# Performance work log

Measured on AMD Instinct MI355X. Metric: run time of the kernel, lower is better.

## Reference

```python
import jax, jax.numpy as jnp
import numpy as np

# pywt db4 decomposition low-pass filter
_DEC_LO = jnp.array([-0.010597401785069032, 0.0328830116668852, 0.030841381835560764,
                     -0.18703481171909309, -0.027983769416859854, 0.6308807679298589,
                     0.7148465705529157, 0.2303778133088965], dtype=jnp.float32)
_L = 8
_SIGN = jnp.where(jnp.arange(_L) % 2 == 0, -1.0, 1.0).astype(jnp.float32)
_DEC_HI = _SIGN * _DEC_LO[::-1]            # QMF: dec_hi[k] = (-1)^(k+1) dec_lo[L-1-k]
_REC_LO = _DEC_LO[::-1]
_REC_HI = _DEC_HI[::-1]
_LEVELS = 4


def _conv_valid(x, f):
    # x: [N, n]; true convolution (filter flipped), valid part
    k = f[::-1][None, None, :]
    return jax.lax.conv_general_dilated(x[:, None, :], k, (1,), 'VALID',
                                        dimension_numbers=('NCH', 'OIH', 'NCH'))[:, 0, :]


def _dwt(x):
    # one symmetric-mode DWT level; x: [N, n] -> (cA, cD) each [N, (n+L-1)//2]
    xp = jnp.pad(x, ((0, 0), (_L - 1, _L - 1)), mode='symmetric')
    return _conv_valid(xp, _DEC_LO)[:, 1::2], _conv_valid(xp, _DEC_HI)[:, 1::2]


def _idwt(a, d):
    # inverse DWT level; a,d: [N, m] -> [N, 2m-L+2]
    m = a.shape[-1]
    up_a = jnp.zeros((a.shape[0], 2 * m - 1), a.dtype).at[:, ::2].set(a)
    up_d = jnp.zeros((d.shape[0], 2 * m - 1), d.dtype).at[:, ::2].set(d)
    y = (_conv_valid(jnp.pad(up_a, ((0, 0), (_L - 1, _L - 1))), _REC_LO)
         + _conv_valid(jnp.pad(up_d, ((0, 0), (_L - 1, _L - 1))), _REC_HI))
    return y[:, _L - 2: y.shape[-1] - (_L - 2)]


def _wavelet_compress(x, level):
    # batched equivalent of the per-(b,c) pywt wavedec/threshold/waverec loop
    B, C, T = x.shape
    a = x.reshape(B * C, T)
    details = []
    for _ in range(_LEVELS):
        a, d = _dwt(a)
        details.append(d)
    thr = level * jnp.std(a, axis=-1, keepdims=True)  # np.std (ddof=0) of approx coeffs per row
    hard = lambda c: jnp.where(jnp.abs(c) < thr, jnp.zeros((), c.dtype), c)
    a = hard(a)
    for d in reversed(details):
        d = hard(d)
        if a.shape[-1] > d.shape[-1]:
            a = a[:, :d.shape[-1]]  # pywt waverec length alignment
        a = _idwt(a, d)
    if a.shape[-1] >= T:
        a = a[:, :T]
    else:
        a = jnp.pad(a, ((0, 0), (0, T - a.shape[-1])))
    return a.reshape(B, C, T)


def _spectral_distortion(x, key, freq_mask_prob=0.3, time_mask_prob=0.3):
    T = x.shape[-1]
    k1, k2, k3, k4 = jax.random.split(key, 4)
    X = jnp.fft.fft(x, axis=-1)
    mag, ph = jnp.abs(X), jnp.angle(X)
    idx = jnp.arange(T)
    fw = int(0.1 * T)
    f0 = jax.random.randint(k2, (), 0, T - fw)
    apply_f = jax.random.uniform(k1, ()) < freq_mask_prob
    fmask = apply_f & (idx >= f0) & (idx < f0 + fw)
    mag = mag * jnp.where(fmask, 0.1, 1.0).astype(mag.dtype)
    xd = jnp.fft.ifft(mag * jnp.exp(1j * ph), axis=-1).real.astype(x.dtype)
    tw = int(0.05 * T)
    t0 = jax.random.randint(k4, (), 0, T - tw)
    apply_t = jax.random.uniform(k3, ()) < time_mask_prob
    tmask = apply_t & (idx >= t0) & (idx < t0 + tw)
    return xd * jnp.where(tmask, 0.1, 1.0).astype(x.dtype)


def _add_noise(x, key, noise_std=0.02):
    # torch.std is unbiased -> ddof=1
    noise = jax.random.normal(key, x.shape, x.dtype) * noise_std * jnp.std(x, axis=-1, keepdims=True, ddof=1)
    return x + noise


def setup_inputs() -> dict:
    key = jax.random.key(0)
    x = jax.random.normal(key, (64, 64, 4096), dtype=jnp.float32)
    return {"x": x}


def reference(x):
    compression_level = 0.5  # fixed draw from compression_levels for determinism
    kd, kn, kcd, kcn = jax.random.split(jax.random.key(42), 4)
    compressed = _wavelet_compress(x, compression_level)
    distorted = _spectral_distortion(x, kd)
    noisy = _add_noise(x, kn)
    comb = _wavelet_compress(x, compression_level * 0.5)
    comb = _spectral_distortion(comb, kcd)
    comb = _add_noise(comb, kcn)
    # views: original, compressed, distorted, noisy, combined
    return (x, compressed, distorted, noisy, comb)
```

## Files before the change

### kernel.cpp

```cpp
#include <hip/hip_runtime.h>
#include <stdint.h>

#define T_LEN 4096
#define N_ROWS 4096
#define N_ELEM (4096u * 4096u)
#define PD(i) ((i) + ((i) >> 5))

__constant__ float c_DEC_LO[8] = {
  -0.010597401785069032f, 0.0328830116668852f, 0.030841381835560764f,
  -0.18703481171909309f, -0.027983769416859854f, 0.6308807679298589f,
   0.7148465705529157f, 0.2303778133088965f };
__constant__ float c_DEC_HI[8] = {
  -0.2303778133088965f, 0.7148465705529157f, -0.6308807679298589f,
  -0.027983769416859854f, 0.18703481171909309f, 0.030841381835560764f,
  -0.0328830116668852f, -0.010597401785069032f };

#define RL0 0.2303778133088965f
#define RL1 0.7148465705529157f
#define RL2 0.6308807679298589f
#define RL3 (-0.027983769416859854f)
#define RL4 (-0.18703481171909309f)
#define RL5 0.030841381835560764f
#define RL6 0.0328830116668852f
#define RL7 (-0.010597401785069032f)
#define RH0 (-0.010597401785069032f)
#define RH1 (-0.0328830116668852f)
#define RH2 0.030841381835560764f
#define RH3 0.18703481171909309f
#define RH4 (-0.027983769416859854f)
#define RH5 (-0.6308807679298589f)
#define RH6 0.7148465705529157f
#define RH7 (-0.2303778133088965f)

__host__ __device__ __forceinline__ uint32_t rotl32(uint32_t v, int r) {
  return (v << r) | (v >> (32 - r));
}

__host__ __device__ __forceinline__ void tf2x32(uint32_t k0, uint32_t k1,
                                                uint32_t c0, uint32_t c1,
                                                uint32_t& o0, uint32_t& o1) {
  uint32_t ks2 = k0 ^ k1 ^ 0x1BD11BDAu;
  uint32_t x0 = c0 + k0;
  uint32_t x1 = c1 + k1;
#define TFR(r) { x0 += x1; x1 = rotl32(x1, r); x1 ^= x0; }
  TFR(13) TFR(15) TFR(26) TFR(6)
  x0 += k1;  x1 += ks2 + 1u;
  TFR(17) TFR(29) TFR(16) TFR(24)
  x0 += ks2; x1 += k0 + 2u;
  TFR(13) TFR(15) TFR(26) TFR(6)
  x0 += k0;  x1 += k1 + 3u;
  TFR(17) TFR(29) TFR(16) TFR(24)
  x0 += k1;  x1 += ks2 + 4u;
  TFR(13) TFR(15) TFR(26) TFR(6)
  x0 += ks2; x1 += k0 + 5u;
#undef TFR
  o0 = x0; o1 = x1;
}

__host__ __device__ __forceinline__ uint32_t jbits_scalar(uint32_t kx, uint32_t ky) {
  uint32_t a, b; tf2x32(kx, ky, 0u, 0u, a, b);
  return a ^ b;
}

__device__ __forceinline__ uint32_t jbits_elem(uint32_t kx, uint32_t ky, uint32_t i) {
  uint32_t a, b; tf2x32(kx, ky, 0u, i, a, b); return a ^ b;
}

__host__ __device__ __forceinline__ float junif_scalar(uint32_t kx, uint32_t ky) {
  union { uint32_t u; float f; } cv;
  cv.u = (jbits_scalar(kx, ky) >> 9) | 0x3f800000u;
  return cv.f - 1.0f;
}

__host__ __device__ __forceinline__ void jsplit2(uint32_t kx, uint32_t ky, uint32_t* o) {
  tf2x32(kx, ky, 0u, 0u, o[0], o[1]);
  tf2x32(kx, ky, 0u, 1u, o[2], o[3]);
}

__host__ __device__ __forceinline__ void jsplit4(uint32_t kx, uint32_t ky, uint32_t* o) {
  tf2x32(kx, ky, 0u, 0u, o[0], o[1]);
  tf2x32(kx, ky, 0u, 1u, o[2], o[3]);
  tf2x32(kx, ky, 0u, 2u, o[4], o[5]);
  tf2x32(kx, ky, 0u, 3u, o[6], o[7]);
}

__host__ __device__ __forceinline__ int jrandint(uint32_t kx, uint32_t ky, uint32_t span) {
  uint32_t c[4];
  jsplit2(kx, ky, c);
  uint32_t hi = jbits_scalar(c[0], c[1]);
  uint32_t lo = jbits_scalar(c[2], c[3]);
  uint32_t mult = 65536u % span;
  mult = (mult * mult) % span;
  uint32_t off = ((hi % span) * mult + (lo % span)) % span;
  return (int)off;
}

__host__ __device__ void distort_params(uint32_t kx, uint32_t ky,
                                        int* f0, int* af, int* t0, int* at) {
  uint32_t q[8];
  jsplit4(kx, ky, q);
  *af = junif_scalar(q[0], q[1]) < 0.3f;
  *f0 = jrandint(q[2], q[3], 3687u);
  *at = junif_scalar(q[4], q[5]) < 0.3f;
  *t0 = jrandint(q[6], q[7], 3892u);
}

__device__ __forceinline__ float erfinv32(float x) {
  float w = -log1pf(-x * x);
  float p;
  if (w < 5.0f) {
    w = w - 2.5f;
    p = 2.81022636e-08f;
    p = fmaf(p, w, 3.43273939e-07f);
    p = fmaf(p, w, -3.5233877e-06f);
    p = fmaf(p, w, -4.39150654e-06f);
    p = fmaf(p, w, 0.00021858087f);
    p = fmaf(p, w, -0.00125372503f);
    p = fmaf(p, w, -0.00417768164f);
    p = fmaf(p, w, 0.246640727f);
    p = fmaf(p, w, 1.50140941f);
  } else {
    w = sqrtf(w) - 3.0f;
    p = -0.000200214257f;
    p = fmaf(p, w, 0.000100950558f);
    p = fmaf(p, w, 0.00134934322f);
    p = fmaf(p, w, -0.00367342844f);
    p = fmaf(p, w, 0.00573950773f);
    p = fmaf(p, w, -0.0076224613f);
    p = fmaf(p, w, 0.00943887047f);
    p = fmaf(p, w, 1.00167406f);
    p = fmaf(p, w, 2.83297682f);
  }
  return p * x;
}

__device__ __forceinline__ float jax_normal_from_bits(uint32_t bits) {
  union { uint32_t u; float f; } cv;
  cv.u = (bits >> 9) | 0x3f800000u;
  float f = cv.f - 1.0f;
  const float lo = -0.99999994f;
  float u = __fadd_rn(__fmul_rn(f, 2.0f), lo);
  u = fmaxf(lo, u);
  return 1.41421356f * erfinv32(u);
}

__device__ __forceinline__ float tree8(const float* p) {
  return __fadd_rn(
      __fadd_rn(__fadd_rn(p[0], p[1]), __fadd_rn(p[2], p[3])),
      __fadd_rn(__fadd_rn(p[4], p[5]), __fadd_rn(p[6], p[7])));
}

__device__ __forceinline__ void dwt_one(const float* a, int n, int i,
                                        float* oA, float* oD) {
  int base = 2 * i - 6;
  float pa[8], pd[8];
  #pragma unroll
  for (int j = 0; j < 8; ++j) {
    int q = base + j;
    q = (q < 0) ? (-q - 1) : ((q >= n) ? (2 * n - 1 - q) : q);
    float xv = a[q];
    pa[j] = __fmul_rn(c_DEC_LO[7 - j], xv);
    pd[j] = __fmul_rn(c_DEC_HI[7 - j], xv);
  }
  *oA = tree8(pa); *oD = tree8(pd);
}

__device__ __forceinline__ void dwt_chunk4(const float* a, int i0,
                                           float* oa, float* od) {
  const float4* ap = reinterpret_cast<const float4*>(a + 2 * i0 - 8);
  float4 v0 = ap[0], v1 = ap[1], v2 = ap[2], v3 = ap[3];
  float x[16] = {v0.x, v0.y, v0.z, v0.w, v1.x, v1.y, v1.z, v1.w,
                 v2.x, v2.y, v2.z, v2.w, v3.x, v3.y, v3.z, v3.w};
  float ra[4], rd[4];
  #pragma unroll
  for (int p = 0; p < 4; ++p) {
    float pa[8], pd[8];
    #pragma unroll
    for (int j = 0; j < 8; ++j) {
      float xv = x[2 * p + 2 + j];
      pa[j] = __fmul_rn(c_DEC_LO[7 - j], xv);
      pd[j] = __fmul_rn(c_DEC_HI[7 - j], xv);
    }
    ra[p] = tree8(pa); rd[p] = tree8(pd);
  }
  *reinterpret_cast<float4*>(&oa[i0]) = make_float4(ra[0], ra[1], ra[2], ra[3]);
  *reinterpret_cast<float4*>(&od[i0]) = make_float4(rd[0], rd[1], rd[2], rd[3]);
}

__device__ void dwt_step(const float* a, int n, float* oa, float* od,
                         int nOut, int tid) {
  int iHi = (n - 2) >> 1;
  int nPair = nOut >> 1;
  for (int u = tid; u < nPair; u += 256) {
    int i0 = 2 * u;
    if (u >= 2 && (i0 + 1) <= iHi) {
      int base = 2 * i0 - 6;
      float x[10];
      #pragma unroll
      for (int j = 0; j < 10; ++j) x[j] = a[base + j];
      float p0[8], p1[8], q0[8], q1[8];
      #pragma unroll
      for (int j = 0; j < 8; ++j) {
        p0[j] = __fmul_rn(c_DEC_LO[7 - j], x[j]);
        q0[j] = __fmul_rn(c_DEC_HI[7 - j], x[j]);
        p1[j] = __fmul_rn(c_DEC_LO[7 - j], x[j + 2]);
        q1[j] = __fmul_rn(c_DEC_HI[7 - j], x[j + 2]);
      }
      *reinterpret_cast<float2*>(&oa[i0]) = make_float2(tree8(p0), tree8(p1));
      *reinterpret_cast<float2*>(&od[i0]) = make_float2(tree8(q0), tree8(q1));
    } else {
      float a0, d0, a1, d1;
      dwt_one(a, n, i0, &a0, &d0);
      dwt_one(a, n, i0 + 1, &a1, &d1);
      oa[i0] = a0; od[i0] = d0;
      oa[i0 + 1] = a1; od[i0 + 1] = d1;
    }
  }
  for (int i = 2 * nPair + tid; i < nOut; i += 256) {
    float av, dv;
    dwt_one(a, n, i, &av, &dv);
    oa[i] = av; od[i] = dv;
  }
}

__device__ __forceinline__ void idwt_pair_vals(const float* __restrict__ a,
                                               const float* __restrict__ d,
                                               int h, float thr, bool trA,
                                               float* ev, float* ov) {
  float a0 = a[h], a1 = a[h + 1], a2 = a[h + 2], a3 = a[h + 3];
  if (trA) {
    a0 = (fabsf(a0) < thr) ? 0.f : a0;
    a1 = (fabsf(a1) < thr) ? 0.f : a1;
    a2 = (fabsf(a2) < thr) ? 0.f : a2;
    a3 = (fabsf(a3) < thr) ? 0.f : a3;
  }
  float d0 = d[h], d1 = d[h + 1], d2 = d[h + 2], d3 = d[h + 3];
  d0 = (fabsf(d0) < thr) ? 0.f : d0;
  d1 = (fabsf(d1) < thr) ? 0.f : d1;
  d2 = (fabsf(d2) < thr) ? 0.f : d2;
  d3 = (fabsf(d3) < thr) ? 0.f : d3;
  float saE = __fadd_rn(__fadd_rn(__fmul_rn(RL6, a0), __fmul_rn(RL4, a1)),
                        __fadd_rn(__fmul_rn(RL2, a2), __fmul_rn(RL0, a3)));
  float sdE = __fadd_rn(__fadd_rn(__fmul_rn(RH6, d0), __fmul_rn(RH4, d1)),
                        __fadd_rn(__fmul_rn(RH2, d2), __fmul_rn(RH0, d3)));
  float saO = __fadd_rn(__fadd_rn(__fmul_rn(RL7, a0), __fmul_rn(RL5, a1)),
                        __fadd_rn(__fmul_rn(RL3, a2), __fmul_rn(RL1, a3)));
  float sdO = __fadd_rn(__fadd_rn(__fmul_rn(RH7, d0), __fmul_rn(RH5, d1)),
                        __fadd_rn(__fmul_rn(RH3, d2), __fmul_rn(RH1, d3)));
  *ev = __fadd_rn(saE, sdE);
  *ov = __fadd_rn(saO, sdO);
}

__device__ __forceinline__ void idwt_chunk4(const float* __restrict__ a,
                                            const float* __restrict__ d,
                                            int h0, float thr, bool trA,
                                            float* o8) {
  float4 va0 = *reinterpret_cast<const float4*>(a + h0);
  float4 va1 = *reinterpret_cast<const float4*>(a + h0 + 4);
  float4 vd0 = *reinterpret_cast<const float4*>(d + h0);
  float4 vd1 = *reinterpret_cast<const float4*>(d + h0 + 4);
  float A8[8] = {va0.x, va0.y, va0.z, va0.w, va1.x, va1.y, va1.z, va1.w};
  float D8[8] = {vd0.x, vd0.y, vd0.z, vd0.w, vd1.x, vd1.y, vd1.z, vd1.w};
  if (trA) {
    #pragma unroll
    for (int j = 0; j < 8; ++j) A8[j] = (fabsf(A8[j]) < thr) ? 0.f : A8[j];
  }
  #pragma unroll
  for (int j = 0; j < 8; ++j) D8[j] = (fabsf(D8[j]) < thr) ? 0.f : D8[j];
  #pragma unroll
  for (int p = 0; p < 4; ++p) {
    float a0 = A8[p], a1 = A8[p + 1], a2 = A8[p + 2], a3 = A8[p + 3];
    float d0 = D8[p], d1 = D8[p + 1], d2 = D8[p + 2], d3 = D8[p + 3];
    float saE = __fadd_rn(__fadd_rn(__fmul_rn(RL6, a0), __fmul_rn(RL4, a1)),
                          __fadd_rn(__fmul_rn(RL2, a2), __fmul_rn(RL0, a3)));
    float sdE = __fadd_rn(__fadd_rn(__fmul_rn(RH6, d0), __fmul_rn(RH4, d1)),
                          __fadd_rn(__fmul_rn(RH2, d2), __fmul_rn(RH0, d3)));
    float saO = __fadd_rn(__fadd_rn(__fmul_rn(RL7, a0), __fmul_rn(RL5, a1)),
                          __fadd_rn(__fmul_rn(RL3, a2), __fmul_rn(RL1, a3)));
    float sdO = __fadd_rn(__fadd_rn(__fmul_rn(RH7, d0), __fmul_rn(RH5, d1)),
                          __fadd_rn(__fmul_rn(RH3, d2), __fmul_rn(RH1, d3)));
    o8[2 * p]     = __fadd_rn(saE, sdE);
    o8[2 * p + 1] = __fadd_rn(saO, sdO);
  }
}

__device__ void idwt_step(const float* __restrict__ a, const float* __restrict__ d,
                          float* __restrict__ out, int nOut, float thr,
                          bool trA, int tid) {
  int nPair = nOut >> 1;
  for (int h = tid; h < nPair; h += 256) {
    float ev, ov;
    idwt_pair_vals(a, d, h, thr, trA, &ev, &ov);
    *reinterpret_cast<float2*>(&out[2 * h]) = make_float2(ev, ov);
  }
  if (nOut & 1) {
    int h = nPair;
    if (tid == (h & 255)) {
      float ev, ov;
      idwt_pair_vals(a, d, h, thr, trA, &ev, &ov);
      out[2 * h] = ev;
    }
  }
}

__device__ void np_pw262_partials(const float* src, float* pbuf, int tid) {
  if (tid < 24) {
    int blk = tid >> 3, k = tid & 7;
    const float* base = src + (blk == 0 ? 0 : (blk == 1 ? 128 : 192));
    int iters = (blk == 0 ? 16 : 8);
    float r = base[k];
    for (int it = 1; it < iters; ++it) r = __fadd_rn(r, base[8 * it + k]);
    pbuf[tid] = r;
  }
}

__device__ float np_pw262_combine(const float* src, const float* pbuf) {
  float b0 = tree8(pbuf + 0);
  float b1 = tree8(pbuf + 8);
  float b2 = tree8(pbuf + 16);
  for (int i = 256; i < 262; ++i) b2 = __fadd_rn(b2, src[i]);
  return __fadd_rn(b0, __fadd_rn(b1, b2));
}

__global__ __launch_bounds__(256, 4)
void wavelet_kernel(const float* __restrict__ x, float* __restrict__ out0,
                    float* __restrict__ out1, float* __restrict__ out4,
                    int fuse, int at_c, int t0_c, uint32_t kcx, uint32_t kcy) {
  extern __shared__ float smem[];
  float* A  = smem;
  float* B  = smem + 4096;
  float* D1 = smem + 6148;
  float* D2 = smem + 8200;
  float* D3 = smem + 9230;
  float* D4 = smem + 9748;
  float* SC = smem + 10010;
  float* Bp = B + 512;
  const int row = blockIdx.x, tid = threadIdx.x;
  const float4* s4 = reinterpret_cast<const float4*>(x + (size_t)row * T_LEN);
  float4* o04 = reinterpret_cast<float4*>(out0 + (size_t)row * T_LEN);
  #pragma unroll
  for (int k = 0; k < 4; ++k) {
    float4 v = s4[tid + (k << 8)];
    *reinterpret_cast<float4*>(&A[4 * (tid + (k << 8))]) = v;
    o04[tid + (k << 8)] = v;
  }
  __syncthreads();

  if (tid == 0) {
    #pragma unroll
    for (int i = 0; i < 4; ++i) {
      float av, dv; dwt_one(A, 4096, i, &av, &dv); B[i] = av; D1[i] = dv;
    }
  } else {
    dwt_chunk4(A, 4 * tid, B, D1);
  }
  dwt_chunk4(A, 1024 + 4 * tid, B, D1);
  if (tid < 3) {
    float av, dv; dwt_one(A, 4096, 2048 + tid, &av, &dv);
    B[2048 + tid] = av; D1[2048 + tid] = dv;
  }
  __syncthreads();

  if (tid == 0) {
    #pragma unroll
    for (int i = 0; i < 4; ++i) {
      float av, dv; dwt_one(B, 2051, i, &av, &dv); A[i] = av; D2[i] = dv;
    }
  } else {
    dwt_chunk4(B, 4 * tid, A, D2);
  }
  if (tid < 5) {
    float av, dv; dwt_one(B, 2051, 1024 + tid, &av, &dv);
    A[1024 + tid] = av; D2[1024 + tid] = dv;
  }
  __syncthreads();

  dwt_step(A, 1029, B, D3, 518, tid);  __syncthreads();
  dwt_step(B, 518, A, D4, 262, tid);   __syncthreads();

  np_pw262_partials(A, Bp, tid);
  __syncthreads();
  if (tid == 0) SC[0] = np_pw262_combine(A, Bp) / 262.0f;
  __syncthreads();
  float mu = SC[0];
  for (int i = tid; i < 262; i += 256) {
    float dv = __fsub_rn(A[i], mu);
    B[i] = __fmul_rn(dv, dv);
  }
  __syncthreads();
  np_pw262_partials(B, Bp, tid);
  __syncthreads();
  if (tid == 0) SC[1] = __fsqrt_rn(np_pw262_combine(B, Bp) / 262.0f);
  __syncthreads();
  float sigma = SC[1];

  float ra0 = A[tid];
  float ra1 = (tid < 6) ? A[256 + tid] : 0.f;

  {
    float thr = __fmul_rn(0.5f, sigma);
    idwt_step(A, D4, B, 518, thr, true, tid);   __syncthreads();
    idwt_step(B, D3, A, 1029, thr, false, tid); __syncthreads();
    {
      float o8[8];
      idwt_chunk4(A, D2, 4 * tid, thr, false, o8);
      *reinterpret_cast<float4*>(&B[8 * tid])     = make_float4(o8[0], o8[1], o8[2], o8[3]);
      *reinterpret_cast<float4*>(&B[8 * tid + 4]) = make_float4(o8[4], o8[5], o8[6], o8[7]);
      if (tid == 0) {
        float ev, ov;
        idwt_pair_vals(A, D2, 1024, thr, false, &ev, &ov);
        B[2048] = ev; B[2049] = ov;
      } else if (tid == 1) {
        float ev, ov;
        idwt_pair_vals(A, D2, 1025, thr, false, &ev, &ov);
        B[2050] = ev;
      }
    }
    __syncthreads();
    float* dstRow = out1 + (size_t)row * T_LEN;
    float o8[8];
    idwt_chunk4(B, D1, 4 * tid, thr, false, o8);
    *reinterpret_cast<float4*>(&dstRow[8 * tid])     = make_float4(o8[0], o8[1], o8[2], o8[3]);
    *reinterpret_cast<float4*>(&dstRow[8 * tid + 4]) = make_float4(o8[4], o8[5], o8[6], o8[7]);
    idwt_chunk4(B, D1, 1024 + 4 * tid, thr, false, o8);
    *reinterpret_cast<float4*>(&dstRow[2048 + 8 * tid])     = make_float4(o8[0], o8[1], o8[2], o8[3]);
    *reinterpret_cast<float4*>(&dstRow[2048 + 8 * tid + 4]) = make_float4(o8[4], o8[5], o8[6], o8[7]);
  }
  __syncthreads();
  A[tid] = ra0;
  if (tid < 6) A[256 + tid] = ra1;
  __syncthreads();

  float thr = __fmul_rn(0.25f, sigma);
  idwt_step(A, D4, B, 518, thr, true, tid);   __syncthreads();
  idwt_step(B, D3, A, 1029, thr, false, tid); __syncthreads();
  {
    float o8[8];
    idwt_chunk4(A, D2, 4 * tid, thr, false, o8);
    *reinterpret_cast<float4*>(&B[8 * tid])     = make_float4(o8[0], o8[1], o8[2], o8[3]);
    *reinterpret_cast<float4*>(&B[8 * tid + 4]) = make_float4(o8[4], o8[5], o8[6], o8[7]);
    if (tid == 0) {
      float ev, ov;
      idwt_pair_vals(A, D2, 1024, thr, false, &ev, &ov);
      B[2048] = ev; B[2049] = ov;
    } else if (tid == 1) {
      float ev, ov;
      idwt_pair_vals(A, D2, 1025, thr, false, &ev, &ov);
      B[2050] = ev;
    }
  }
  __syncthreads();

  float* dstRow = out4 + (size_t)row * T_LEN;
  if (!fuse) {
    float o8[8];
    idwt_chunk4(B, D1, 4 * tid, thr, false, o8);
    *reinterpret_cast<float4*>(&dstRow[8 * tid])     = make_float4(o8[0], o8[1], o8[2], o8[3]);
    *reinterpret_cast<float4*>(&dstRow[8 * tid + 4]) = make_float4(o8[4], o8[5], o8[6], o8[7]);
    idwt_chunk4(B, D1, 1024 + 4 * tid, thr, false, o8);
    *reinterpret_cast<float4*>(&dstRow[2048 + 8 * tid])     = make_float4(o8[0], o8[1], o8[2], o8[3]);
    *reinterpret_cast<float4*>(&dstRow[2048 + 8 * tid + 4]) = make_float4(o8[4], o8[5], o8[6], o8[7]);
    return;
  }

  float w[16];
  idwt_chunk4(B, D1, 4 * tid, thr, false, w);
  idwt_chunk4(B, D1, 1024 + 4 * tid, thr, false, w + 8);
  if (at_c) {
    #pragma unroll
    for (int i = 0; i < 16; ++i) {
      int col = (i < 8) ? (8 * tid + i) : (2048 + 8 * tid + (i - 8));
      if (col >= t0_c && col < t0_c + 204) w[i] *= 0.1f;
    }
  }
  __syncthreads();
  float* red = B;
  float acc = 0.f;
  #pragma unroll
  for (int i = 0; i < 16; ++i) acc += w[i];
  red[tid] = acc; __syncthreads();
  for (int o = 128; o > 0; o >>= 1) { if (tid < o) red[tid] += red[tid + o]; __syncthreads(); }
  float nmu = red[0] * (1.0f / 4096.0f);
  __syncthreads();
  acc = 0.f;
  #pragma unroll
  for (int i = 0; i < 16; ++i) { float dv = w[i] - nmu; acc += dv * dv; }
  red[tid] = acc; __syncthreads();
  for (int o = 128; o > 0; o >>= 1) { if (tid < o) red[tid] += red[tid + o]; __syncthreads(); }
  float nsig = sqrtf(red[0] / 4095.0f);

  float ov[16];
  #pragma unroll
  for (int i = 0; i < 16; ++i) {
    uint32_t col = (uint32_t)((i < 8) ? (8 * tid + i) : (2048 + 8 * tid + (i - 8)));
    uint32_t idx = ((uint32_t)row << 12) + col;
    float z = jax_normal_from_bits(jbits_elem(kcx, kcy, idx));
    ov[i] = w[i] + __fmul_rn(__fmul_rn(z, 0.02f), nsig);
  }
  *reinterpret_cast<float4*>(&dstRow[8 * tid])            = make_float4(ov[0], ov[1], ov[2], ov[3]);
  *reinterpret_cast<float4*>(&dstRow[8 * tid + 4])        = make_float4(ov[4], ov[5], ov[6], ov[7]);
  *reinterpret_cast<float4*>(&dstRow[2048 + 8 * tid])     = make_float4(ov[8], ov[9], ov[10], ov[11]);
  *reinterpret_cast<float4*>(&dstRow[2048 + 8 * tid + 4]) = make_float4(ov[12], ov[13], ov[14], ov[15]);
}

__constant__ int c_STW2_OFF[5] = {0, 512, 640, 672, 680};

__device__ __forceinline__ int rev2048(int k) {
  return ((k & 3) << 9) | (((k >> 2) & 3) << 7) | (((k >> 4) & 3) << 5)
       | (((k >> 6) & 3) << 3) | (((k >> 8) & 3) << 1) | (k >> 10);
}

__device__ __forceinline__ float maskP(int K, int f0) {
  float m1 = (K >= f0 && K < f0 + 409) ? 0.1f : 1.0f;
  int K2 = (4096 - K) & 4095;
  float m2 = (K2 >= f0 && K2 < f0 + 409) ? 0.1f : 1.0f;
  return 0.5f * (m1 + m2);
}

__device__ __forceinline__ void retangle_one(int k, int f0,
    float zkr, float zki, float zmr, float zmi, float* outr, float* outi) {
  float xer = 0.5f * (zkr + zmr), xei = 0.5f * (zki - zmi);
  float xor_ = 0.5f * (zki + zmi), xoi = 0.5f * (zmr - zkr);
  float sn, cs;
  __sincosf((float)k * (-1.5339807878856412e-3f), &sn, &cs);
  float wxr = xor_ * cs - xoi * sn, wxi = xor_ * sn + xoi * cs;
  float X1r = xer + wxr, X1i = xei + wxi;
  float X2r = xer - wxr, X2i = xei - wxi;
  float m1 = maskP(k, f0), m2 = maskP(k + 2048, f0);
  X1r *= m1; X1i *= m1; X2r *= m2; X2i *= m2;
  float yer = 0.5f * (X1r + X2r), yei = 0.5f * (X1i + X2i);
  float dr = 0.5f * (X1r - X2r), di = 0.5f * (X1i - X2i);
  float yor = dr * cs + di * sn, yoi = di * cs - dr * sn;
  *outr = yer - yoi; *outi = yei + yor;
}

__device__ void distort_core(float* smem, const float4* v4, float* w,
                             int af, int f0, int at, int t0, int tid) {
  float* RE = smem;
  float* IM = smem + 2112;
  float2* STW = (float2*)(smem + 4224);
  if (af) {
    for (int t = tid; t < 682; t += 256) {
      int s, j;
      if (t < 512) { s = 0; j = t; }
      else if (t < 640) { s = 1; j = t - 512; }
      else if (t < 672) { s = 2; j = t - 640; }
      else if (t < 680) { s = 3; j = t - 672; }
      else { s = 4; j = t - 680; }
      int e = j << (2 * s);
      float ang = (float)e * (-3.0679615757712823e-3f);
      float sn, cs;
      __sincosf(ang, &sn, &cs);
      STW[t] = make_float2(cs, sn);
    }
    #pragma unroll
    for (int k = 0; k < 4; ++k) {
      int n = 2 * (tid + (k << 8));
      RE[PD(n)]     = v4[k].x; IM[PD(n)]     = v4[k].y;
      RE[PD(n + 1)] = v4[k].z; IM[PD(n + 1)] = v4[k].w;
    }
    __syncthreads();
    for (int s = 0; s < 5; ++s) {
      int Lsh = 11 - 2 * s, Qsh = Lsh - 2, Qm = (1 << Qsh) - 1, off = c_STW2_OFF[s];
      for (int b = tid; b < 512; b += 256) {
        int j = b & Qm, g = b >> Qsh;
        int i0 = (g << Lsh) + j;
        int i1 = i0 + (1 << Qsh), i2 = i1 + (1 << Qsh), i3 = i2 + (1 << Qsh);
        float x0r = RE[PD(i0)], x0i = IM[PD(i0)];
        float x1r = RE[PD(i1)], x1i = IM[PD(i1)];
        float x2r = RE[PD(i2)], x2i = IM[PD(i2)];
        float x3r = RE[PD(i3)], x3i = IM[PD(i3)];
        float t0r = x0r + x2r, t0i = x0i + x2i;
        float t1r = x0r - x2r, t1i = x0i - x2i;
        float t2r = x1r + x3r, t2i = x1i + x3i;
        float t3r = x1r - x3r, t3i = x1i - x3i;
        float2 w1 = STW[off + j];
        float c1 = w1.x, s1 = w1.y;
        float c2 = c1 * c1 - s1 * s1, s2 = 2.f * c1 * s1;
        float c3 = c1 * c2 - s1 * s2, s3 = c1 * s2 + s1 * c2;
        RE[PD(i0)] = t0r + t2r; IM[PD(i0)] = t0i + t2i;
        float u1r = t1r + t3i, u1i = t1i - t3r;
        RE[PD(i1)] = u1r * c1 - u1i * s1; IM[PD(i1)] = u1r * s1 + u1i * c1;
        float u2r = t0r - t2r, u2i = t0i - t2i;
        RE[PD(i2)] = u2r * c2 - u2i * s2; IM[PD(i2)] = u2r * s2 + u2i * c2;
        float u3r = t1r - t3i, u3i = t1i + t3r;
        RE[PD(i3)] = u3r * c3 - u3i * s3; IM[PD(i3)] = u3r * s3 + u3i * c3;
      }
      __syncthreads();
    }
    for (int m = tid; m < 1024; m += 256) {
      int i0 = 2 * m, i1 = 2 * m + 1;
      float ar = RE[PD(i0)], ai = IM[PD(i0)];
      float br = RE[PD(i1)], bi = IM[PD(i1)];
      RE[PD(i0)] = ar + br; IM[PD(i0)] = ai + bi;
      RE[PD(i1)] = ar - br; IM[PD(i1)] = ai - bi;
    }
    __syncthreads();
    for (int k0 = tid; k0 < 1024; k0 += 256) {
      if (k0 == 0) {
        {
          int pk = PD(rev2048(0));
          float zr = RE[pk], zi = IM[pk], orr, oi;
          retangle_one(0, f0, zr, zi, zr, zi, &orr, &oi);
          RE[pk] = orr; IM[pk] = oi;
        }
        {
          int pk = PD(rev2048(1024));
          float zr = RE[pk], zi = IM[pk], orr, oi;
          retangle_one(1024, f0, zr, zi, zr, zi, &orr, &oi);
          RE[pk] = orr; IM[pk] = oi;
        }
      } else {
        int m = 2048 - k0;
        int pk = PD(rev2048(k0)), pm = PD(rev2048(m));
        float zkr = RE[pk], zki = IM[pk];
        float zmr = RE[pm], zmi = IM[pm];
        float akr, aki, amr, ami;
        retangle_one(k0, f0, zkr, zki, zmr, zmi, &akr, &aki);
        retangle_one(m, f0, zmr, zmi, zkr, zki, &amr, &ami);
        RE[pk] = akr; IM[pk] = aki;
        RE[pm] = amr; IM[pm] = ami;
      }
    }
    __syncthreads();
    for (int m = tid; m < 1024; m += 256) {
      int i0 = 2 * m, i1 = 2 * m + 1;
      float ar = RE[PD(i0)], ai = IM[PD(i0)];
      float br = RE[PD(i1)], bi = IM[PD(i1)];
      RE[PD(i0)] = ar + br; IM[PD(i0)] = ai + bi;
      RE[PD(i1)] = ar - br; IM[PD(i1)] = ai - bi;
    }
    __syncthreads();
    for (int s = 4; s >= 0; --s) {
      int Lsh = 11 - 2 * s, Qsh = Lsh - 2, Qm = (1 << Qsh) - 1, off = c_STW2_OFF[s];
      for (int b = tid; b < 512; b += 256) {
        int j = b & Qm, g = b >> Qsh;
        int i0 = (g << Lsh) + j;
        int i1 = i0 + (1 << Qsh), i2 = i1 + (1 << Qsh), i3 = i2 + (1 << Qsh);
        float y0r = RE[PD(i0)], y0i = IM[PD(i0)];
        float y1r = RE[PD(i1)], y1i = IM[PD(i1)];
        float y2r = RE[PD(i2)], y2i = IM[PD(i2)];
        float y3r = RE[PD(i3)], y3i = IM[PD(i3)];
        float2 w1 = STW[off + j];
        float c1 = w1.x, s1 = -w1.y;
        float c2 = c1 * c1 - s1 * s1, s2 = 2.f * c1 * s1;
        float c3 = c1 * c2 - s1 * s2, s3 = c1 * s2 + s1 * c2;
        float z1r = y1r * c1 - y1i * s1, z1i = y1r * s1 + y1i * c1;
        float z2r = y2r * c2 - y2i * s2, z2i = y2r * s2 + y2i * c2;
        float z3r = y3r * c3 - y3i * s3, z3i = y3r * s3 + y3i * c3;
        float u0r = y0r + z2r, u0i = y0i + z2i;
        float u2r = y0r - z2r, u2i = y0i - z2i;
        float u1r = z1r + z3r, u1i = z1i + z3i;
        float u3r = z3i - z1i, u3i = z1r - z3r;
        RE[PD(i0)] = u0r + u1r; IM[PD(i0)] = u0i + u1i;
        RE[PD(i1)] = u2r + u3r; IM[PD(i1)] = u2i + u3i;
        RE[PD(i2)] = u0r - u1r; IM[PD(i2)] = u0i - u1i;
        RE[PD(i3)] = u2r - u3r; IM[PD(i3)] = u2i - u3i;
      }
      __syncthreads();
    }
    #pragma unroll
    for (int k = 0; k < 4; ++k) {
      int n = 2 * (tid + (k << 8));
      w[4 * k + 0] = RE[PD(n)]     * (1.0f / 2048.0f);
      w[4 * k + 1] = IM[PD(n)]     * (1.0f / 2048.0f);
      w[4 * k + 2] = RE[PD(n + 1)] * (1.0f / 2048.0f);
      w[4 * k + 3] = IM[PD(n + 1)] * (1.0f / 2048.0f);
    }
    __syncthreads();
  } else {
    #pragma unroll
    for (int k = 0; k < 4; ++k) {
      w[4 * k + 0] = v4[k].x; w[4 * k + 1] = v4[k].y;
      w[4 * k + 2] = v4[k].z; w[4 * k + 3] = v4[k].w;
    }
  }
  if (at) {
    #pragma unroll
    for (int i = 0; i < 16; ++i) {
      int col = 4 * (tid + ((i >> 2) << 8)) + (i & 3);
      if (col >= t0 && col < t0 + 204) w[i] *= 0.1f;
    }
  }
}

__global__ __launch_bounds__(256)
void distort_noise_kernel(const float* __restrict__ src, float* __restrict__ dst_d,
                          float* __restrict__ dst_n,
                          int af, int f0, int at, int t0, int nod, int wd,
                          uint32_t kx, uint32_t ky) {
  extern __shared__ float smem[];
  const int row = blockIdx.x, tid = threadIdx.x;

  const float4* s4 = reinterpret_cast<const float4*>(src + (size_t)row * T_LEN);
  float4 v4[4];
  #pragma unroll
  for (int k = 0; k < 4; ++k) v4[k] = s4[tid + (k << 8)];

  float w[16];
  distort_core(smem, v4, w, af, f0, at, t0, tid);

  if (wd) {
    float4* d4 = reinterpret_cast<float4*>(dst_d + (size_t)row * T_LEN);
    #pragma unroll
    for (int k = 0; k < 4; ++k)
      d4[tid + (k << 8)] = make_float4(w[4 * k], w[4 * k + 1], w[4 * k + 2], w[4 * k + 3]);
  }

  float nv[16];
  #pragma unroll
  for (int i = 0; i < 16; ++i) {
    float q;
    if (nod) q = w[i];
    else {
      float4 vv = v4[i >> 2];
      q = (i & 3) == 0 ? vv.x : (i & 3) == 1 ? vv.y : (i & 3) == 2 ? vv.z : vv.w;
    }
    nv[i] = q;
  }
  float* red = smem;
  float acc = 0.f;
  #pragma unroll
  for (int i = 0; i < 16; ++i) acc += nv[i];
  red[tid] = acc; __syncthreads();
  for (int o = 128; o > 0; o >>= 1) { if (tid < o) red[tid] += red[tid + o]; __syncthreads(); }
  float mu = red[0] * (1.0f / 4096.0f);
  __syncthreads();
  acc = 0.f;
  #pragma unroll
  for (int i = 0; i < 16; ++i) { float dv = nv[i] - mu; acc += dv * dv; }
  red[tid] = acc; __syncthreads();
  for (int o = 128; o > 0; o >>= 1) { if (tid < o) red[tid] += red[tid + o]; __syncthreads(); }
  float sigma = sqrtf(red[0] / 4095.0f);

  float4* n4 = reinterpret_cast<float4*>(dst_n + (size_t)row * T_LEN);
  #pragma unroll
  for (int k = 0; k < 4; ++k) {
    float o[4];
    #pragma unroll
    for (int c = 0; c < 4; ++c) {
      uint32_t col = (uint32_t)(4 * (tid + (k << 8)) + c);
      uint32_t idx = ((uint32_t)row << 12) + col;
      float z = jax_normal_from_bits(jbits_elem(kx, ky, idx));
      o[c] = nv[4 * k + c] + __fmul_rn(__fmul_rn(z, 0.02f), sigma);
    }
    n4[tid + (k << 8)] = make_float4(o[0], o[1], o[2], o[3]);
  }
}

extern "C" void kernel_launch(void* const* d_in, const int* in_sizes, int n_in,
                              void* d_out, int out_size, void* d_ws, size_t ws_size,
                              hipStream_t stream) {
  const float* x = (const float*)d_in[0];
  float* out = (float*)d_out;
  float* o0 = out;
  float* o1 = out + (size_t)N_ELEM;
  float* o2 = out + 2 * (size_t)N_ELEM;
  float* o3 = out + 3 * (size_t)N_ELEM;
  float* o4 = out + 4 * (size_t)N_ELEM;

  uint32_t r[8];
  jsplit4(0u, 42u, r);
  int f0d, afd, t0d, atd, f0c, afc, t0c, atc;
  distort_params(r[0], r[1], &f0d, &afd, &t0d, &atd);
  distort_params(r[4], r[5], &f0c, &afc, &t0c, &atc);

  const size_t WAVE_LDS = 10012u * 4u;
  const size_t FFT_LDS  = 5588u * 4u;

  hipLaunchKernelGGL(wavelet_kernel, dim3(N_ROWS), dim3(256), WAVE_LDS, stream,
                     x, o0, o1, o4, afc ? 0 : 1, atc, t0c, r[6], r[7]);
  hipLaunchKernelGGL(distort_noise_kernel, dim3(N_ROWS), dim3(256),
                     afd ? FFT_LDS : 1024, stream,
                     x, o2, o3, afd, f0d, atd, t0d, 0, 1, r[2], r[3]);
  if (afc) {
    hipLaunchKernelGGL(distort_noise_kernel, dim3(N_ROWS), dim3(256), FFT_LDS, stream,
                       o4, o4, o4, 1, f0c, atc, t0c, 1, 0, r[6], r[7]);
  }
}
```

Baseline: 273.7 us.

## Run both threshold reconstructions together in one interleaved inverse-DWT pass

Result: faster. 267.1 us (-2.4%).

```diff
diff --git a/kernel.cpp b/kernel.cpp
--- a/kernel.cpp
+++ b/kernel.cpp
@@ -223,22 +223,9 @@
   }
 }
 
-__device__ __forceinline__ void idwt_pair_vals(const float* __restrict__ a,
-                                               const float* __restrict__ d,
-                                               int h, float thr, bool trA,
-                                               float* ev, float* ov) {
-  float a0 = a[h], a1 = a[h + 1], a2 = a[h + 2], a3 = a[h + 3];
-  if (trA) {
-    a0 = (fabsf(a0) < thr) ? 0.f : a0;
-    a1 = (fabsf(a1) < thr) ? 0.f : a1;
-    a2 = (fabsf(a2) < thr) ? 0.f : a2;
-    a3 = (fabsf(a3) < thr) ? 0.f : a3;
-  }
-  float d0 = d[h], d1 = d[h + 1], d2 = d[h + 2], d3 = d[h + 3];
-  d0 = (fabsf(d0) < thr) ? 0.f : d0;
-  d1 = (fabsf(d1) < thr) ? 0.f : d1;
-  d2 = (fabsf(d2) < thr) ? 0.f : d2;
-  d3 = (fabsf(d3) < thr) ? 0.f : d3;
+__device__ __forceinline__ void idwt_core(float a0, float a1, float a2, float a3,
+                                          float d0, float d1, float d2, float d3,
+                                          float* ev, float* ov) {
   float saE = __fadd_rn(__fadd_rn(__fmul_rn(RL6, a0), __fmul_rn(RL4, a1)),
                         __fadd_rn(__fmul_rn(RL2, a2), __fmul_rn(RL0, a3)));
   float sdE = __fadd_rn(__fadd_rn(__fmul_rn(RH6, d0), __fmul_rn(RH4, d1)),
@@ -251,56 +238,99 @@
   *ov = __fadd_rn(saO, sdO);
 }
 
-__device__ __forceinline__ void idwt_chunk4(const float* __restrict__ a,
-                                            const float* __restrict__ d,
-                                            int h0, float thr, bool trA,
-                                            float* o8) {
-  float4 va0 = *reinterpret_cast<const float4*>(a + h0);
-  float4 va1 = *reinterpret_cast<const float4*>(a + h0 + 4);
-  float4 vd0 = *reinterpret_cast<const float4*>(d + h0);
-  float4 vd1 = *reinterpret_cast<const float4*>(d + h0 + 4);
-  float A8[8] = {va0.x, va0.y, va0.z, va0.w, va1.x, va1.y, va1.z, va1.w};
-  float D8[8] = {vd0.x, vd0.y, vd0.z, vd0.w, vd1.x, vd1.y, vd1.z, vd1.w};
-  if (trA) {
-    #pragma unroll
-    for (int j = 0; j < 8; ++j) A8[j] = (fabsf(A8[j]) < thr) ? 0.f : A8[j];
-  }
-  #pragma unroll
-  for (int j = 0; j < 8; ++j) D8[j] = (fabsf(D8[j]) < thr) ? 0.f : D8[j];
-  #pragma unroll
-  for (int p = 0; p < 4; ++p) {
-    float a0 = A8[p], a1 = A8[p + 1], a2 = A8[p + 2], a3 = A8[p + 3];
-    float d0 = D8[p], d1 = D8[p + 1], d2 = D8[p + 2], d3 = D8[p + 3];
-    float saE = __fadd_rn(__fadd_rn(__fmul_rn(RL6, a0), __fmul_rn(RL4, a1)),
-                          __fadd_rn(__fmul_rn(RL2, a2), __fmul_rn(RL0, a3)));
-    float sdE = __fadd_rn(__fadd_rn(__fmul_rn(RH6, d0), __fmul_rn(RH4, d1)),
-                          __fadd_rn(__fmul_rn(RH2, d2), __fmul_rn(RH0, d3)));
-    float saO = __fadd_rn(__fadd_rn(__fmul_rn(RL7, a0), __fmul_rn(RL5, a1)),
-                          __fadd_rn(__fmul_rn(RL3, a2), __fmul_rn(RL1, a3)));
-    float sdO = __fadd_rn(__fadd_rn(__fmul_rn(RH7, d0), __fmul_rn(RH5, d1)),
-                          __fadd_rn(__fmul_rn(RH3, d2), __fmul_rn(RH1, d3)));
-    o8[2 * p]     = __fadd_rn(saE, sdE);
-    o8[2 * p + 1] = __fadd_rn(saO, sdO);
-  }
-}
-
-__device__ void idwt_step(const float* __restrict__ a, const float* __restrict__ d,
-                          float* __restrict__ out, int nOut, float thr,
-                          bool trA, int tid) {
+#define TH(v, t) ((fabsf(v) < (t)) ? 0.f : (v))
+
+__device__ void idwt_dual_step(const float* __restrict__ a0b,
+                               const float* __restrict__ a1b,
+                               const float* __restrict__ d,
+                               float* __restrict__ o0b, float* __restrict__ o1b,
+                               int nOut, float thr0, float thr1, bool trA, int tid) {
   int nPair = nOut >> 1;
   for (int h = tid; h < nPair; h += 256) {
-    float ev, ov;
-    idwt_pair_vals(a, d, h, thr, trA, &ev, &ov);
-    *reinterpret_cast<float2*>(&out[2 * h]) = make_float2(ev, ov);
+    float dd0 = d[h], dd1 = d[h + 1], dd2 = d[h + 2], dd3 = d[h + 3];
+    {
+      float a0 = a0b[h], a1 = a0b[h + 1], a2 = a0b[h + 2], a3 = a0b[h + 3];
+      if (trA) { a0 = TH(a0, thr0); a1 = TH(a1, thr0); a2 = TH(a2, thr0); a3 = TH(a3, thr0); }
+      float ev, ov;
+      idwt_core(a0, a1, a2, a3, TH(dd0, thr0), TH(dd1, thr0), TH(dd2, thr0), TH(dd3, thr0), &ev, &ov);
+      *reinterpret_cast<float2*>(&o0b[2 * h]) = make_float2(ev, ov);
+    }
+    {
+      float a0 = a1b[h], a1 = a1b[h + 1], a2 = a1b[h + 2], a3 = a1b[h + 3];
+      if (trA) { a0 = TH(a0, thr1); a1 = TH(a1, thr1); a2 = TH(a2, thr1); a3 = TH(a3, thr1); }
+      float ev, ov;
+      idwt_core(a0, a1, a2, a3, TH(dd0, thr1), TH(dd1, thr1), TH(dd2, thr1), TH(dd3, thr1), &ev, &ov);
+      *reinterpret_cast<float2*>(&o1b[2 * h]) = make_float2(ev, ov);
+    }
   }
   if (nOut & 1) {
     int h = nPair;
     if (tid == (h & 255)) {
-      float ev, ov;
-      idwt_pair_vals(a, d, h, thr, trA, &ev, &ov);
-      out[2 * h] = ev;
-    }
-  }
+      float dd0 = d[h], dd1 = d[h + 1], dd2 = d[h + 2], dd3 = d[h + 3];
+      {
+        float a0 = a0b[h], a1 = a0b[h + 1], a2 = a0b[h + 2], a3 = a0b[h + 3];
+        if (trA) { a0 = TH(a0, thr0); a1 = TH(a1, thr0); a2 = TH(a2, thr0); a3 = TH(a3, thr0); }
+        float ev, ov;
+        idwt_core(a0, a1, a2, a3, TH(dd0, thr0), TH(dd1, thr0), TH(dd2, thr0), TH(dd3, thr0), &ev, &ov);
+        o0b[2 * h] = ev;
+      }
+      {
+        float a0 = a1b[h], a1 = a1b[h + 1], a2 = a1b[h + 2], a3 = a1b[h + 3];
+        if (trA) { a0 = TH(a0, thr1); a1 = TH(a1, thr1); a2 = TH(a2, thr1); a3 = TH(a3, thr1); }
+        float ev, ov;
+        idwt_core(a0, a1, a2, a3, TH(dd0, thr1), TH(dd1, thr1), TH(dd2, thr1), TH(dd3, thr1), &ev, &ov);
+        o1b[2 * h] = ev;
+      }
+    }
+  }
+}
+
+__device__ __forceinline__ void idwt_dual_chunk4(const float* __restrict__ a0b,
+                                                 const float* __restrict__ a1b,
+                                                 const float* __restrict__ d,
+                                                 int h0, float thr0, float thr1,
+                                                 float* o8v0, float* o8v1) {
+  float4 vd0 = *reinterpret_cast<const float4*>(d + h0);
+  float4 vd1 = *reinterpret_cast<const float4*>(d + h0 + 4);
+  float D8[8] = {vd0.x, vd0.y, vd0.z, vd0.w, vd1.x, vd1.y, vd1.z, vd1.w};
+  {
+    float4 va0 = *reinterpret_cast<const float4*>(a0b + h0);
+    float4 va1 = *reinterpret_cast<const float4*>(a0b + h0 + 4);
+    float A8[8] = {va0.x, va0.y, va0.z, va0.w, va1.x, va1.y, va1.z, va1.w};
+    float T8[8];
+    #pragma unroll
+    for (int j = 0; j < 8; ++j) T8[j] = TH(D8[j], thr0);
+    #pragma unroll
+    for (int p = 0; p < 4; ++p) {
+      idwt_core(A8[p], A8[p + 1], A8[p + 2], A8[p + 3],
+                T8[p], T8[p + 1], T8[p + 2], T8[p + 3],
+                &o8v0[2 * p], &o8v0[2 * p + 1]);
+    }
+  }
+  {
+    float4 va0 = *reinterpret_cast<const float4*>(a1b + h0);
+    float4 va1 = *reinterpret_cast<const float4*>(a1b + h0 + 4);
+    float A8[8] = {va0.x, va0.y, va0.z, va0.w, va1.x, va1.y, va1.z, va1.w};
+    float T8[8];
+    #pragma unroll
+    for (int j = 0; j < 8; ++j) T8[j] = TH(D8[j], thr1);
+    #pragma unroll
+    for (int p = 0; p < 4; ++p) {
+      idwt_core(A8[p], A8[p + 1], A8[p + 2], A8[p + 3],
+                T8[p], T8[p + 1], T8[p + 2], T8[p + 3],
+                &o8v1[2 * p], &o8v1[2 * p + 1]);
+    }
+  }
+}
+
+__device__ __forceinline__ void idwt_pair_vals(const float* __restrict__ a,
+                                               const float* __restrict__ d,
+                                               int h, float thr,
+                                               float* ev, float* ov) {
+  float a0 = a[h], a1 = a[h + 1], a2 = a[h + 2], a3 = a[h + 3];
+  float d0 = TH(d[h], thr), d1 = TH(d[h + 1], thr);
+  float d2 = TH(d[h + 2], thr), d3 = TH(d[h + 3], thr);
+  idwt_core(a0, a1, a2, a3, d0, d1, d2, d3, ev, ov);
 }
 
 __device__ void np_pw262_partials(const float* src, float* pbuf, int tid) {
@@ -327,21 +357,29 @@
                     float* __restrict__ out1, float* __restrict__ out4,
                     int fuse, int at_c, int t0_c, uint32_t kcx, uint32_t kcy) {
   extern __shared__ float smem[];
-  float* A  = smem;
-  float* B  = smem + 4096;
-  float* D1 = smem + 6148;
-  float* D2 = smem + 8200;
-  float* D3 = smem + 9230;
-  float* D4 = smem + 9748;
-  float* SC = smem + 10010;
-  float* Bp = B + 512;
+  float* P  = smem;
+  float* Q  = smem + 4116;
+  float* D1 = smem + 6180;
+  float* D2 = smem + 8232;
+  float* D3 = smem + 9264;
+  float* D4 = smem + 9784;
+  float* SC = smem + 10048;
+  float* Bp = smem + 10052;
+  float* L3 = P + 1536;
+  float* A4 = P + 2560;
+  float* P0 = P;
+  float* P1 = P + 1032;
+  float* Q0 = Q;
+  float* Q1 = Q + 520;
+  float* V0 = Q;
+  float* V1 = P + 2064;
   const int row = blockIdx.x, tid = threadIdx.x;
   const float4* s4 = reinterpret_cast<const float4*>(x + (size_t)row * T_LEN);
   float4* o04 = reinterpret_cast<float4*>(out0 + (size_t)row * T_LEN);
   #pragma unroll
   for (int k = 0; k < 4; ++k) {
     float4 v = s4[tid + (k << 8)];
-    *reinterpret_cast<float4*>(&A[4 * (tid + (k << 8))]) = v;
+    *reinterpret_cast<float4*>(&P[4 * (tid + (k << 8))]) = v;
     o04[tid + (k << 8)] = v;
   }
   __syncthreads();
@@ -349,123 +387,104 @@
   if (tid == 0) {
     #pragma unroll
     for (int i = 0; i < 4; ++i) {
-      float av, dv; dwt_one(A, 4096, i, &av, &dv); B[i] = av; D1[i] = dv;
+      float av, dv; dwt_one(P, 4096, i, &av, &dv); Q[i] = av; D1[i] = dv;
     }
   } else {
-    dwt_chunk4(A, 4 * tid, B, D1);
-  }
-  dwt_chunk4(A, 1024 + 4 * tid, B, D1);
+    dwt_chunk4(P, 4 * tid, Q, D1);
+  }
+  dwt_chunk4(P, 1024 + 4 * tid, Q, D1);
   if (tid < 3) {
-    float av, dv; dwt_one(A, 4096, 2048 + tid, &av, &dv);
-    B[2048 + tid] = av; D1[2048 + tid] = dv;
+    float av, dv; dwt_one(P, 4096, 2048 + tid, &av, &dv);
+    Q[2048 + tid] = av; D1[2048 + tid] = dv;
   }
   __syncthreads();
 
   if (tid == 0) {
     #pragma unroll
     for (int i = 0; i < 4; ++i) {
-      float av, dv; dwt_one(B, 2051, i, &av, &dv); A[i] = av; D2[i] = dv;
+      float av, dv; dwt_one(Q, 2051, i, &av, &dv); P[i] = av; D2[i] = dv;
     }
   } else {
-    dwt_chunk4(B, 4 * tid, A, D2);
+    dwt_chunk4(Q, 4 * tid, P, D2);
   }
   if (tid < 5) {
-    float av, dv; dwt_one(B, 2051, 1024 + tid, &av, &dv);
-    A[1024 + tid] = av; D2[1024 + tid] = dv;
-  }
-  __syncthreads();
-
-  dwt_step(A, 1029, B, D3, 518, tid);  __syncthreads();
-  dwt_step(B, 518, A, D4, 262, tid);   __syncthreads();
-
-  np_pw262_partials(A, Bp, tid);
-  __syncthreads();
-  if (tid == 0) SC[0] = np_pw262_combine(A, Bp) / 262.0f;
+    float av, dv; dwt_one(Q, 2051, 1024 + tid, &av, &dv);
+    P[1024 + tid] = av; D2[1024 + tid] = dv;
+  }
+  __syncthreads();
+
+  dwt_step(P, 1029, L3, D3, 518, tid);  __syncthreads();
+  dwt_step(L3, 518, A4, D4, 262, tid);  __syncthreads();
+
+  np_pw262_partials(A4, Bp, tid);
+  __syncthreads();
+  if (tid == 0) SC[0] = np_pw262_combine(A4, Bp) / 262.0f;
   __syncthreads();
   float mu = SC[0];
   for (int i = tid; i < 262; i += 256) {
-    float dv = __fsub_rn(A[i], mu);
-    B[i] = __fmul_rn(dv, dv);
-  }
-  __syncthreads();
-  np_pw262_partials(B, Bp, tid);
-  __syncthreads();
-  if (tid == 0) SC[1] = __fsqrt_rn(np_pw262_combine(B, Bp) / 262.0f);
+    float dv = __fsub_rn(A4[i], mu);
+    Q[i] = __fmul_rn(dv, dv);
+  }
+  __syncthreads();
+  np_pw262_partials(Q, Bp, tid);
+  __syncthreads();
+  if (tid == 0) SC[1] = __fsqrt_rn(np_pw262_combine(Q, Bp) / 262.0f);
   __syncthreads();
   float sigma = SC[1];
-
-  float ra0 = A[tid];
-  float ra1 = (tid < 6) ? A[256 + tid] : 0.f;
-
+  float thr0 = __fmul_rn(0.5f, sigma);
+  float thr1 = __fmul_rn(0.25f, sigma);
+
+  idwt_dual_step(A4, A4, D4, Q0, Q1, 518, thr0, thr1, true, tid);
+  __syncthreads();
+  idwt_dual_step(Q0, Q1, D3, P0, P1, 1029, thr0, thr1, false, tid);
+  __syncthreads();
   {
-    float thr = __fmul_rn(0.5f, sigma);
-    idwt_step(A, D4, B, 518, thr, true, tid);   __syncthreads();
-    idwt_step(B, D3, A, 1029, thr, false, tid); __syncthreads();
-    {
-      float o8[8];
-      idwt_chunk4(A, D2, 4 * tid, thr, false, o8);
-      *reinterpret_cast<float4*>(&B[8 * tid])     = make_float4(o8[0], o8[1], o8[2], o8[3]);
-      *reinterpret_cast<float4*>(&B[8 * tid + 4]) = make_float4(o8[4], o8[5], o8[6], o8[7]);
-      if (tid == 0) {
-        float ev, ov;
-        idwt_pair_vals(A, D2, 1024, thr, false, &ev, &ov);
-        B[2048] = ev; B[2049] = ov;
-      } else if (tid == 1) {
-        float ev, ov;
-        idwt_pair_vals(A, D2, 1025, thr, false, &ev, &ov);
-        B[2050] = ev;
-      }
-    }
-    __syncthreads();
-    float* dstRow = out1 + (size_t)row * T_LEN;
-    float o8[8];
-    idwt_chunk4(B, D1, 4 * tid, thr, false, o8);
-    *reinterpret_cast<float4*>(&dstRow[8 * tid])     = make_float4(o8[0], o8[1], o8[2], o8[3]);
-    *reinterpret_cast<float4*>(&dstRow[8 * tid + 4]) = make_float4(o8[4], o8[5], o8[6], o8[7]);
-    idwt_chunk4(B, D1, 1024 + 4 * tid, thr, false, o8);
-    *reinterpret_cast<float4*>(&dstRow[2048 + 8 * tid])     = make_float4(o8[0], o8[1], o8[2], o8[3]);
-    *reinterpret_cast<float4*>(&dstRow[2048 + 8 * tid + 4]) = make_float4(o8[4], o8[5], o8[6], o8[7]);
-  }
-  __syncthreads();
-  A[tid] = ra0;
-  if (tid < 6) A[256 + tid] = ra1;
-  __syncthreads();
-
-  float thr = __fmul_rn(0.25f, sigma);
-  idwt_step(A, D4, B, 518, thr, true, tid);   __syncthreads();
-  idwt_step(B, D3, A, 1029, thr, false, tid); __syncthreads();
-  {
-    float o8[8];
-    idwt_chunk4(A, D2, 4 * tid, thr, false, o8);
-    *reinterpret_cast<float4*>(&B[8 * tid])     = make_float4(o8[0], o8[1], o8[2], o8[3]);
-    *reinterpret_cast<float4*>(&B[8 * tid + 4]) = make_float4(o8[4], o8[5], o8[6], o8[7]);
+    float o80[8], o81[8];
+    idwt_dual_chunk4(P0, P1, D2, 4 * tid, thr0, thr1, o80, o81);
+    *reinterpret_cast<float4*>(&V0[8 * tid])     = make_float4(o80[0], o80[1], o80[2], o80[3]);
+    *reinterpret_cast<float4*>(&V0[8 * tid + 4]) = make_float4(o80[4], o80[5], o80[6], o80[7]);
+    *reinterpret_cast<float4*>(&V1[8 * tid])     = make_float4(o81[0], o81[1], o81[2], o81[3]);
+    *reinterpret_cast<float4*>(&V1[8 * tid + 4]) = make_float4(o81[4], o81[5], o81[6], o81[7]);
     if (tid == 0) {
       float ev, ov;
-      idwt_pair_vals(A, D2, 1024, thr, false, &ev, &ov);
-      B[2048] = ev; B[2049] = ov;
+      idwt_pair_vals(P0, D2, 1024, thr0, &ev, &ov);
+      V0[2048] = ev; V0[2049] = ov;
+      idwt_pair_vals(P1, D2, 1024, thr1, &ev, &ov);
+      V1[2048] = ev; V1[2049] = ov;
     } else if (tid == 1) {
       float ev, ov;
-      idwt_pair_vals(A, D2, 1025, thr, false, &ev, &ov);
-      B[2050] = ev;
-    }
-  }
-  __syncthreads();
-
-  float* dstRow = out4 + (size_t)row * T_LEN;
+      idwt_pair_vals(P0, D2, 1025, thr0, &ev, &ov);
+      V0[2050] = ev;
+      idwt_pair_vals(P1, D2, 1025, thr1, &ev, &ov);
+      V1[2050] = ev;
+    }
+  }
+  __syncthreads();
+
+  float* o1Row = out1 + (size_t)row * T_LEN;
+  float* o4Row = out4 + (size_t)row * T_LEN;
+  float w[16];
+  {
+    float o80[8], o81[8];
+    idwt_dual_chunk4(V0, V1, D1, 4 * tid, thr0, thr1, o80, o81);
+    *reinterpret_cast<float4*>(&o1Row[8 * tid])     = make_float4(o80[0], o80[1], o80[2], o80[3]);
+    *reinterpret_cast<float4*>(&o1Row[8 * tid + 4]) = make_float4(o80[4], o80[5], o80[6], o80[7]);
+    #pragma unroll
+    for (int j = 0; j < 8; ++j) w[j] = o81[j];
+    idwt_dual_chunk4(V0, V1, D1, 1024 + 4 * tid, thr0, thr1, o80, o81);
+    *reinterpret_cast<float4*>(&o1Row[2048 + 8 * tid])     = make_float4(o80[0], o80[1], o80[2], o80[3]);
+    *reinterpret_cast<float4*>(&o1Row[2048 + 8 * tid + 4]) = make_float4(o80[4], o80[5], o80[6], o80[7]);
+    #pragma unroll
+    for (int j = 0; j < 8; ++j) w[8 + j] = o81[j];
+  }
   if (!fuse) {
-    float o8[8];
-    idwt_chunk4(B, D1, 4 * tid, thr, false, o8);
-    *reinterpret_cast<float4*>(&dstRow[8 * tid])     = make_float4(o8[0], o8[1], o8[2], o8[3]);
-    *reinterpret_cast<float4*>(&dstRow[8 * tid + 4]) = make_float4(o8[4], o8[5], o8[6], o8[7]);
-    idwt_chunk4(B, D1, 1024 + 4 * tid, thr, false, o8);
-    *reinterpret_cast<float4*>(&dstRow[2048 + 8 * tid])     = make_float4(o8[0], o8[1], o8[2], o8[3]);
-    *reinterpret_cast<float4*>(&dstRow[2048 + 8 * tid + 4]) = make_float4(o8[4], o8[5], o8[6], o8[7]);
+    *reinterpret_cast<float4*>(&o4Row[8 * tid])            = make_float4(w[0], w[1], w[2], w[3]);
+    *reinterpret_cast<float4*>(&o4Row[8 * tid + 4])        = make_float4(w[4], w[5], w[6], w[7]);
+    *reinterpret_cast<float4*>(&o4Row[2048 + 8 * tid])     = make_float4(w[8], w[9], w[10], w[11]);
+    *reinterpret_cast<float4*>(&o4Row[2048 + 8 * tid + 4]) = make_float4(w[12], w[13], w[14], w[15]);
     return;
   }
 
-  float w[16];
-  idwt_chunk4(B, D1, 4 * tid, thr, false, w);
-  idwt_chunk4(B, D1, 1024 + 4 * tid, thr, false, w + 8);
   if (at_c) {
     #pragma unroll
     for (int i = 0; i < 16; ++i) {
@@ -474,7 +493,7 @@
     }
   }
   __syncthreads();
-  float* red = B;
+  float* red = Q;
   float acc = 0.f;
   #pragma unroll
   for (int i = 0; i < 16; ++i) acc += w[i];
@@ -497,10 +516,10 @@
     float z = jax_normal_from_bits(jbits_elem(kcx, kcy, idx));
     ov[i] = w[i] + __fmul_rn(__fmul_rn(z, 0.02f), nsig);
   }
-  *reinterpret_cast<float4*>(&dstRow[8 * tid])            = make_float4(ov[0], ov[1], ov[2], ov[3]);
-  *reinterpret_cast<float4*>(&dstRow[8 * tid + 4])        = make_float4(ov[4], ov[5], ov[6], ov[7]);
-  *reinterpret_cast<float4*>(&dstRow[2048 + 8 * tid])     = make_float4(ov[8], ov[9], ov[10], ov[11]);
-  *reinterpret_cast<float4*>(&dstRow[2048 + 8 * tid + 4]) = make_float4(ov[12], ov[13], ov[14], ov[15]);
+  *reinterpret_cast<float4*>(&o4Row[8 * tid])            = make_float4(ov[0], ov[1], ov[2], ov[3]);
+  *reinterpret_cast<float4*>(&o4Row[8 * tid + 4])        = make_float4(ov[4], ov[5], ov[6], ov[7]);
+  *reinterpret_cast<float4*>(&o4Row[2048 + 8 * tid])     = make_float4(ov[8], ov[9], ov[10], ov[11]);
+  *reinterpret_cast<float4*>(&o4Row[2048 + 8 * tid + 4]) = make_float4(ov[12], ov[13], ov[14], ov[15]);
 }
 
 __constant__ int c_STW2_OFF[5] = {0, 512, 640, 672, 680};
@@ -765,7 +784,7 @@
   distort_params(r[0], r[1], &f0d, &afd, &t0d, &atd);
   distort_params(r[4], r[5], &f0c, &afc, &t0c, &atc);
 
-  const size_t WAVE_LDS = 10012u * 4u;
+  const size_t WAVE_LDS = 10076u * 4u;
   const size_t FFT_LDS  = 5588u * 4u;
 
   hipLaunchKernelGGL(wavelet_kernel, dim3(N_ROWS), dim3(256), WAVE_LDS, stream,
```
